# Kernel optimization log

Measured on AMD Instinct MI355X. Metric: run time of the kernel, lower is better.

Reference implementation:

```python
import jax, jax.numpy as jnp
import numpy as np

N, C_IN, H, W = 32, 128, 56, 56
C_OUT, KH, KW = 256, 3, 3
STRIDE = (1, 1)
PAD = (1, 1)


def setup_inputs() -> dict:
    key = jax.random.key(0)
    k_x, k_w, k_b = jax.random.split(key, 3)
    x = jax.random.normal(k_x, (N, C_IN, H, W), dtype=jnp.float32)
    # kaiming_uniform-like scale for weight, uniform bias in [-1/sqrt(fan_in), 1/sqrt(fan_in)]
    fan_in = C_IN * KH * KW
    bound_w = float(np.sqrt(6.0 / ((1 + 5.0) * fan_in)))  # kaiming_uniform a=sqrt(5)
    weight = jax.random.uniform(k_w, (C_OUT, C_IN, KH, KW), dtype=jnp.float32,
                                minval=-bound_w, maxval=bound_w)
    bound_b = float(1.0 / np.sqrt(fan_in))
    bias = jax.random.uniform(k_b, (C_OUT,), dtype=jnp.float32,
                              minval=-bound_b, maxval=bound_b)
    return {"x": x, "weight": weight, "bias": bias}


def reference(x, weight, bias):
    # Faithful math of the im2col conv: zero padding (ph,pw)=(1,1), stride 1,
    # groups=1 -> identical to a standard cross-correlation conv2d + bias.
    out = jax.lax.conv_general_dilated(
        x, weight,
        window_strides=STRIDE,
        padding=[(PAD[0], PAD[0]), (PAD[1], PAD[1])],
        dimension_numbers=("NCHW", "OIHW", "NCHW"),
    )
    return out + bias[None, :, None, None]
```

## Files before the change

### kernel.cpp

```cpp
#include <hip/hip_runtime.h>


#define NB   32
#define CIN  128
#define HH   56
#define WWD  56
#define COUT 256
#define HWP  3136
#define KTOT 1152
#define HP   58
#define XTN  (HP*HP*CIN)

typedef __bf16 bf16x8 __attribute__((ext_vector_type(8)));
typedef float  f32x4  __attribute__((ext_vector_type(4)));
typedef unsigned short u16;
typedef u16 u16x4 __attribute__((ext_vector_type(4)));
typedef u16 u16x8 __attribute__((ext_vector_type(8)));

__device__ __forceinline__ u16 f2b(float f) {
  unsigned u = __float_as_uint(f);
  u += 0x7fffu + ((u >> 16) & 1u);
  return (u16)(u >> 16);
}

__device__ __forceinline__ void load_lds16(const u16* g, u16* l) {
  __builtin_amdgcn_global_load_lds(
      (const __attribute__((address_space(1))) unsigned int*)g,
      (__attribute__((address_space(3))) unsigned int*)l, 16, 0, 0);
}

__global__ __launch_bounds__(256) void k_transpose_x(const float* __restrict__ x,
                                                     u16* __restrict__ xt) {
  __shared__ u16 tile[64][68];
  const int n  = blockIdx.z;
  const int p0 = blockIdx.x * 64;
  const int c0 = blockIdx.y * 64;
  const int t  = threadIdx.x;

  const float* xp = x + (size_t)n * CIN * HWP + (size_t)c0 * HWP + p0;
  const int pl = (t & 15) * 4;
  const int cr = t >> 4;
#pragma unroll
  for (int j = 0; j < 4; ++j) {
    int c = cr + j * 16;
    f32x4 v = *(const f32x4*)&xp[(size_t)c * HWP + pl];
    u16x4 h;
    h[0] = f2b(v[0]); h[1] = f2b(v[1]); h[2] = f2b(v[2]); h[3] = f2b(v[3]);
    *(u16x4*)&tile[c][pl] = h;
  }
  __syncthreads();
  u16* xb = xt + (size_t)n * XTN + c0;
  const int ch = (t & 7) * 8;
  const int pr = t >> 3;
#pragma unroll
  for (int j = 0; j < 2; ++j) {
    int p  = pr + j * 32;
    int s  = p0 + p;
    int oh = s / WWD;
    int ow = s - oh * WWD;
    u16x8 o;
#pragma unroll
    for (int i = 0; i < 8; ++i) o[i] = tile[ch + i][p];
    *(u16x8*)&xb[((size_t)(oh + 1) * HP + (ow + 1)) * CIN + ch] = o;
  }
}

__global__ __launch_bounds__(256) void k_transform_w(const float* __restrict__ w,
                                                     u16* __restrict__ Wt,
                                                     u16* __restrict__ xt) {
  int o = blockIdx.x * 256 + threadIdx.x;
  if (o < COUT * KTOT) {
    int co  = o / KTOT;
    int rem = o - co * KTOT;
    int kk  = rem >> 7;
    int ci  = rem & 127;
    int kh  = kk / 3;
    int kw  = kk - kh * 3;
    Wt[o] = f2b(w[(((size_t)co * CIN + ci) * 3 + kh) * 3 + kw]);
  }
#pragma unroll
  for (int j = 0; j < 4; ++j) {
    unsigned e = (unsigned)o + j * 294912u;
    if (e < 933888u) {
      unsigned n  = e / 29184u;
      unsigned rm = e - n * 29184u;
      unsigned bp = rm >> 7;
      unsigned ch = rm & 127u;
      unsigned ih, iw;
      if (bp < 58u)       { ih = 0;  iw = bp; }
      else if (bp < 116u) { ih = 57; iw = bp - 58u; }
      else { unsigned c2 = bp - 116u; ih = 1u + (c2 >> 1); iw = (c2 & 1u) ? 57u : 0u; }
      xt[(((size_t)n * HP + ih) * HP + iw) * CIN + ch] = (u16)0;
    }
  }
}


#define RD_A(qm_) do { _Pragma("unroll") for (int kk = 0; kk < 2; ++kk) \
    { _Pragma("unroll") for (int ti = 0; ti < 4; ++ti) \
      a[kk][ti] = *(const bf16x8*)&lds[eA + (wm*128 + (qm_)*64 + ti*16 + r)*64 \
                                        + (((kk*4 + q) ^ r7))*8]; } } while (0)

#define RD_B(qn_) do { _Pragma("unroll") for (int kk = 0; kk < 2; ++kk) \
    { _Pragma("unroll") for (int tj = 0; tj < 2; ++tj) \
      b[kk][tj] = *(const bf16x8*)&lds[eB + (wn*64 + (qn_)*32 + tj*16 + r)*64 \
                                        + (((kk*4 + q) ^ r7))*8]; } } while (0)

#define MM(qm_, qn_) do { _Pragma("unroll") for (int kk = 0; kk < 2; ++kk) \
    { _Pragma("unroll") for (int ti = 0; ti < 4; ++ti) \
      { _Pragma("unroll") for (int tj = 0; tj < 2; ++tj) \
        acc[(qm_)*4 + ti][(qn_)*2 + tj] = __builtin_amdgcn_mfma_f32_16x16x32_bf16( \
            a[kk][ti], b[kk][tj], acc[(qm_)*4 + ti][(qn_)*2 + tj], 0, 0, 0); } } } while (0)

__global__ __launch_bounds__(512, 2) void k_conv_gemm(
    const u16* __restrict__ xt, const u16* __restrict__ Wt,
    const float* __restrict__ bias, float* __restrict__ out) {
  extern __shared__ u16 lds[];
  const int tid  = threadIdx.x;
  const int wave = tid >> 6;
  const int lane = tid & 63;
  const int m0   = blockIdx.x * 256;

  const int wm = wave >> 2;
  const int wn = wave & 3;
  const int r  = lane & 15;
  const int q  = lane >> 4;
  const int r7 = r & 7;

  const int rsub = lane >> 3;
  const int ps8  = ((lane & 7) ^ rsub) * 8;

  int pbA[4], pbB[4], ldo[4];
#pragma unroll
  for (int j = 0; j < 4; ++j) {
    const int rowb = wave * 8 + j * 64;
    const int m  = m0 + rowb + rsub;
    const int n  = m / HWP;
    const int s  = m - n * HWP;
    const int oh = s / WWD;
    const int ow = s - oh * WWD;
    pbA[j] = ((n * HP + oh) * HP + ow) * CIN + ps8;
    pbB[j] = (rowb + rsub) * KTOT + ps8;
    ldo[j] = rowb * 64;
  }
  float bias_r[4];
#pragma unroll
  for (int tj = 0; tj < 4; ++tj) bias_r[tj] = bias[wn * 64 + tj * 16 + r];

  f32x4 acc[8][4];
#pragma unroll
  for (int i = 0; i < 8; ++i)
#pragma unroll
    for (int jj = 0; jj < 4; ++jj) acc[i][jj] = (f32x4){0.f, 0.f, 0.f, 0.f};

#pragma unroll
  for (int j = 0; j < 4; ++j) load_lds16(Wt + pbB[j], &lds[49152 + ldo[j]]);
#pragma unroll
  for (int j = 0; j < 4; ++j) load_lds16(xt + pbA[j], &lds[0 + ldo[j]]);
#pragma unroll
  for (int j = 0; j < 4; ++j) load_lds16(xt + pbA[j] + 64, &lds[16384 + ldo[j]]);
  asm volatile("s_waitcnt vmcnt(4)" ::: "memory");
  __builtin_amdgcn_s_barrier();

  bf16x8 a[2][4], b[2][2];
  int bA = 0, bB = 0;

#pragma unroll 1
  for (int kt = 0; kt < 18; ++kt) {
    const int eA  = bA * 16384;
    const int eB  = 49152 + bB * 16384;
    const int sAo = (bA == 0) ? 32768 : (bA - 1) * 16384;
    const int sBo = 49152 + ((bB ^ 1) * 16384);
    const int koffB = (kt + 1) * 64;
    const int kt2  = kt + 2;
    const int ksp2 = kt2 >> 1;
    const int kh2  = (ksp2 >= 6) ? 2 : ((ksp2 >= 3) ? 1 : 0);
    const int kw2  = ksp2 - kh2 * 3;
    const int UA   = (kh2 * HP + kw2) * CIN + ((kt2 & 1) << 6);
    const bool doB = (kt < 17);
    const bool doA = (kt < 16);

    RD_A(0); RD_B(0);
    if (doB) { load_lds16(Wt + pbB[0] + koffB, &lds[sBo + ldo[0]]);
               load_lds16(Wt + pbB[1] + koffB, &lds[sBo + ldo[1]]); }
    __builtin_amdgcn_s_barrier();
    __builtin_amdgcn_s_setprio(1);
    MM(0, 0);
    __builtin_amdgcn_s_setprio(0);
    __builtin_amdgcn_s_barrier();

    RD_B(1);
    if (doB) { load_lds16(Wt + pbB[2] + koffB, &lds[sBo + ldo[2]]);
               load_lds16(Wt + pbB[3] + koffB, &lds[sBo + ldo[3]]); }
    __builtin_amdgcn_s_barrier();
    __builtin_amdgcn_s_setprio(1);
    MM(0, 1);
    __builtin_amdgcn_s_setprio(0);
    __builtin_amdgcn_s_barrier();

    RD_A(1);
    if (doA) { load_lds16(xt + pbA[0] + UA, &lds[sAo + ldo[0]]);
               load_lds16(xt + pbA[1] + UA, &lds[sAo + ldo[1]]); }
    __builtin_amdgcn_s_barrier();
    __builtin_amdgcn_s_setprio(1);
    MM(1, 1);
    __builtin_amdgcn_s_setprio(0);
    __builtin_amdgcn_s_barrier();

    RD_B(0);
    if (doA) { load_lds16(xt + pbA[2] + UA, &lds[sAo + ldo[2]]);
               load_lds16(xt + pbA[3] + UA, &lds[sAo + ldo[3]]); }
    if (kt < 16) { asm volatile("s_waitcnt vmcnt(4)" ::: "memory"); }
    else         { asm volatile("s_waitcnt vmcnt(0)" ::: "memory"); }
    __builtin_amdgcn_s_barrier();
    __builtin_amdgcn_s_setprio(1);
    MM(1, 0);
    __builtin_amdgcn_s_setprio(0);
    __builtin_amdgcn_s_barrier();

    bA = (bA == 2) ? 0 : bA + 1;
    bB ^= 1;
  }

#pragma unroll
  for (int ti = 0; ti < 8; ++ti) {
    const int m4 = m0 + wm * 128 + ti * 16 + q * 4;
    const int n  = m4 / HWP;
    const int s  = m4 - n * HWP;
    float* op = out + (size_t)n * COUT * HWP + s;
#pragma unroll
    for (int tj = 0; tj < 4; ++tj) {
      const int co = wn * 64 + tj * 16 + r;
      f32x4 v = acc[ti][tj];
      const float bv = bias_r[tj];
      v[0] += bv; v[1] += bv; v[2] += bv; v[3] += bv;
      *(f32x4*)(op + (size_t)co * HWP) = v;
    }
  }
}

extern "C" void kernel_launch(void* const* d_in, const int* in_sizes, int n_in,
                              void* d_out, int out_size, void* d_ws, size_t ws_size,
                              hipStream_t stream) {
  const float* x    = (const float*)d_in[0];
  const float* w    = (const float*)d_in[1];
  const float* bias = (const float*)d_in[2];
  float* out        = (float*)d_out;

  u16* xt = (u16*)d_ws;
  u16* Wt = xt + (size_t)NB * XTN;

  static bool attr_done = false;
  if (!attr_done) {
    hipFuncSetAttribute(reinterpret_cast<const void*>(k_conv_gemm),
                        hipFuncAttributeMaxDynamicSharedMemorySize, 163840);
    attr_done = true;
  }

  k_transform_w<<<dim3(1152), dim3(256), 0, stream>>>(w, Wt, xt);
  k_transpose_x<<<dim3(49, 2, 32), dim3(256), 0, stream>>>(x, xt);
  k_conv_gemm<<<dim3(392), dim3(512), 163840, stream>>>(xt, Wt, bias, out);
}
```

Measured before the change: 219.7 us.

## Shrink conv GEMM tiles to 128x128 with simple double-buffered pipeline

Replaces the 256x256-tile, 512-thread conv GEMM (triple-buffered A, 160KB dynamic LDS, fine-grained interleaved barriers and setprio) with 128x128 tiles on 256 threads. It uses a plain two-stage double buffer in 64KB static LDS and a swizzled block-to-tile mapping across 1568 blocks. This is meant to raise occupancy and wave count and simplify scheduling. The cost is less data reuse per tile, roughly doubled global/L2 traffic for X and W, and full vmcnt(0) waits that expose load latency.

```diff
diff --git a/kernel.cpp b/kernel.cpp
--- a/kernel.cpp
+++ b/kernel.cpp
@@ -96,141 +96,109 @@
 }
 
 
-#define RD_A(qm_) do { _Pragma("unroll") for (int kk = 0; kk < 2; ++kk) \
-    { _Pragma("unroll") for (int ti = 0; ti < 4; ++ti) \
-      a[kk][ti] = *(const bf16x8*)&lds[eA + (wm*128 + (qm_)*64 + ti*16 + r)*64 \
-                                        + (((kk*4 + q) ^ r7))*8]; } } while (0)
-
-#define RD_B(qn_) do { _Pragma("unroll") for (int kk = 0; kk < 2; ++kk) \
-    { _Pragma("unroll") for (int tj = 0; tj < 2; ++tj) \
-      b[kk][tj] = *(const bf16x8*)&lds[eB + (wn*64 + (qn_)*32 + tj*16 + r)*64 \
-                                        + (((kk*4 + q) ^ r7))*8]; } } while (0)
-
-#define MM(qm_, qn_) do { _Pragma("unroll") for (int kk = 0; kk < 2; ++kk) \
-    { _Pragma("unroll") for (int ti = 0; ti < 4; ++ti) \
-      { _Pragma("unroll") for (int tj = 0; tj < 2; ++tj) \
-        acc[(qm_)*4 + ti][(qn_)*2 + tj] = __builtin_amdgcn_mfma_f32_16x16x32_bf16( \
-            a[kk][ti], b[kk][tj], acc[(qm_)*4 + ti][(qn_)*2 + tj], 0, 0, 0); } } } while (0)
-
-__global__ __launch_bounds__(512, 2) void k_conv_gemm(
+__device__ __forceinline__ int uX_off(int kt) {
+  int ksp = kt >> 1;
+  int kh  = (ksp >= 6) ? 2 : ((ksp >= 3) ? 1 : 0);
+  int kw  = ksp - kh * 3;
+  return (kh * HP + kw) * CIN + ((kt & 1) << 6);
+}
+
+#define STG(buf_, uxo_, uwo_) do { _Pragma("unroll") \
+  for (int c = 0; c < 4; ++c) { \
+    load_lds16(Wt + pbW[c] + (uwo_), &lW[buf_][ldo[c]]); \
+    load_lds16(xt + pbX[c] + (uxo_), &lX[buf_][ldo[c]]); } } while (0)
+
+#define CMP(buf_) do { _Pragma("unroll") for (int kk = 0; kk < 2; ++kk) { \
+    bf16x8 a[4], b[4]; const int sw = ((kk * 4 + q) ^ r7) * 8; \
+    _Pragma("unroll") for (int ti = 0; ti < 4; ++ti) \
+      a[ti] = *(const bf16x8*)&lX[buf_][(wm + ti * 16 + r) * 64 + sw]; \
+    _Pragma("unroll") for (int tj = 0; tj < 4; ++tj) \
+      b[tj] = *(const bf16x8*)&lW[buf_][(wc + tj * 16 + r) * 64 + sw]; \
+    _Pragma("unroll") for (int ti = 0; ti < 4; ++ti) \
+      _Pragma("unroll") for (int tj = 0; tj < 4; ++tj) \
+        acc[ti][tj] = __builtin_amdgcn_mfma_f32_16x16x32_bf16( \
+            a[ti], b[tj], acc[ti][tj], 0, 0, 0); } } while (0)
+
+__global__ __launch_bounds__(256, 2) void k_conv_gemm(
     const u16* __restrict__ xt, const u16* __restrict__ Wt,
     const float* __restrict__ bias, float* __restrict__ out) {
-  extern __shared__ u16 lds[];
+  __shared__ u16 lW[2][8192];
+  __shared__ u16 lX[2][8192];
+
   const int tid  = threadIdx.x;
   const int wave = tid >> 6;
   const int lane = tid & 63;
-  const int m0   = blockIdx.x * 256;
-
-  const int wm = wave >> 2;
-  const int wn = wave & 3;
+
+  const int bid  = blockIdx.x;
+  const int orig = (bid & 7) * 196 + (bid >> 3);
+  const int by   = orig / 784;
+  const int bx   = orig - by * 784;
+  const int m0   = bx * 128;
+  const int co0  = by * 128;
+
   const int r  = lane & 15;
   const int q  = lane >> 4;
   const int r7 = r & 7;
+  const int wm = (wave & 1) * 64;
+  const int wc = (wave >> 1) * 64;
 
   const int rsub = lane >> 3;
-  const int ps8  = ((lane & 7) ^ rsub) * 8;
-
-  int pbA[4], pbB[4], ldo[4];
-#pragma unroll
-  for (int j = 0; j < 4; ++j) {
-    const int rowb = wave * 8 + j * 64;
+  const int pso  = ((lane & 7) ^ rsub) * 8;
+
+  int pbX[4], pbW[4], ldo[4];
+#pragma unroll
+  for (int c = 0; c < 4; ++c) {
+    const int rowb = wave * 32 + c * 8;
     const int m  = m0 + rowb + rsub;
     const int n  = m / HWP;
     const int s  = m - n * HWP;
     const int oh = s / WWD;
     const int ow = s - oh * WWD;
-    pbA[j] = ((n * HP + oh) * HP + ow) * CIN + ps8;
-    pbB[j] = (rowb + rsub) * KTOT + ps8;
-    ldo[j] = rowb * 64;
+    pbX[c] = ((n * HP + oh) * HP + ow) * CIN + pso;
+    pbW[c] = (co0 + rowb + rsub) * KTOT + pso;
+    ldo[c] = rowb * 64;
   }
   float bias_r[4];
 #pragma unroll
-  for (int tj = 0; tj < 4; ++tj) bias_r[tj] = bias[wn * 64 + tj * 16 + r];
-
-  f32x4 acc[8][4];
-#pragma unroll
-  for (int i = 0; i < 8; ++i)
-#pragma unroll
-    for (int jj = 0; jj < 4; ++jj) acc[i][jj] = (f32x4){0.f, 0.f, 0.f, 0.f};
-
-#pragma unroll
-  for (int j = 0; j < 4; ++j) load_lds16(Wt + pbB[j], &lds[49152 + ldo[j]]);
-#pragma unroll
-  for (int j = 0; j < 4; ++j) load_lds16(xt + pbA[j], &lds[0 + ldo[j]]);
-#pragma unroll
-  for (int j = 0; j < 4; ++j) load_lds16(xt + pbA[j] + 64, &lds[16384 + ldo[j]]);
-  asm volatile("s_waitcnt vmcnt(4)" ::: "memory");
+  for (int tj = 0; tj < 4; ++tj) bias_r[tj] = bias[co0 + wc + tj * 16 + r];
+
+  f32x4 acc[4][4];
+#pragma unroll
+  for (int i = 0; i < 4; ++i)
+#pragma unroll
+    for (int j = 0; j < 4; ++j) acc[i][j] = (f32x4){0.f, 0.f, 0.f, 0.f};
+
+  STG(0, 0, 0);
+  asm volatile("s_waitcnt vmcnt(0)" ::: "memory");
   __builtin_amdgcn_s_barrier();
 
-  bf16x8 a[2][4], b[2][2];
-  int bA = 0, bB = 0;
-
 #pragma unroll 1
-  for (int kt = 0; kt < 18; ++kt) {
-    const int eA  = bA * 16384;
-    const int eB  = 49152 + bB * 16384;
-    const int sAo = (bA == 0) ? 32768 : (bA - 1) * 16384;
-    const int sBo = 49152 + ((bB ^ 1) * 16384);
-    const int koffB = (kt + 1) * 64;
-    const int kt2  = kt + 2;
-    const int ksp2 = kt2 >> 1;
-    const int kh2  = (ksp2 >= 6) ? 2 : ((ksp2 >= 3) ? 1 : 0);
-    const int kw2  = ksp2 - kh2 * 3;
-    const int UA   = (kh2 * HP + kw2) * CIN + ((kt2 & 1) << 6);
-    const bool doB = (kt < 17);
-    const bool doA = (kt < 16);
-
-    RD_A(0); RD_B(0);
-    if (doB) { load_lds16(Wt + pbB[0] + koffB, &lds[sBo + ldo[0]]);
-               load_lds16(Wt + pbB[1] + koffB, &lds[sBo + ldo[1]]); }
+  for (int p = 0; p < 8; ++p) {
+    const int kt = p * 2;
+    STG(1, uX_off(kt + 1), (kt + 1) * 64);
+    CMP(0);
+    asm volatile("s_waitcnt vmcnt(0)" ::: "memory");
     __builtin_amdgcn_s_barrier();
-    __builtin_amdgcn_s_setprio(1);
-    MM(0, 0);
-    __builtin_amdgcn_s_setprio(0);
+    STG(0, uX_off(kt + 2), (kt + 2) * 64);
+    CMP(1);
+    asm volatile("s_waitcnt vmcnt(0)" ::: "memory");
     __builtin_amdgcn_s_barrier();
-
-    RD_B(1);
-    if (doB) { load_lds16(Wt + pbB[2] + koffB, &lds[sBo + ldo[2]]);
-               load_lds16(Wt + pbB[3] + koffB, &lds[sBo + ldo[3]]); }
-    __builtin_amdgcn_s_barrier();
-    __builtin_amdgcn_s_setprio(1);
-    MM(0, 1);
-    __builtin_amdgcn_s_setprio(0);
-    __builtin_amdgcn_s_barrier();
-
-    RD_A(1);
-    if (doA) { load_lds16(xt + pbA[0] + UA, &lds[sAo + ldo[0]]);
-               load_lds16(xt + pbA[1] + UA, &lds[sAo + ldo[1]]); }
-    __builtin_amdgcn_s_barrier();
-    __builtin_amdgcn_s_setprio(1);
-    MM(1, 1);
-    __builtin_amdgcn_s_setprio(0);
-    __builtin_amdgcn_s_barrier();
-
-    RD_B(0);
-    if (doA) { load_lds16(xt + pbA[2] + UA, &lds[sAo + ldo[2]]);
-               load_lds16(xt + pbA[3] + UA, &lds[sAo + ldo[3]]); }
-    if (kt < 16) { asm volatile("s_waitcnt vmcnt(4)" ::: "memory"); }
-    else         { asm volatile("s_waitcnt vmcnt(0)" ::: "memory"); }
-    __builtin_amdgcn_s_barrier();
-    __builtin_amdgcn_s_setprio(1);
-    MM(1, 0);
-    __builtin_amdgcn_s_setprio(0);
-    __builtin_amdgcn_s_barrier();
-
-    bA = (bA == 2) ? 0 : bA + 1;
-    bB ^= 1;
-  }
-
-#pragma unroll
-  for (int ti = 0; ti < 8; ++ti) {
-    const int m4 = m0 + wm * 128 + ti * 16 + q * 4;
+  }
+  STG(1, uX_off(17), 17 * 64);
+  CMP(0);
+  asm volatile("s_waitcnt vmcnt(0)" ::: "memory");
+  __builtin_amdgcn_s_barrier();
+  CMP(1);
+
+#pragma unroll
+  for (int ti = 0; ti < 4; ++ti) {
+    const int m4 = m0 + wm + ti * 16 + q * 4;
     const int n  = m4 / HWP;
     const int s  = m4 - n * HWP;
     float* op = out + (size_t)n * COUT * HWP + s;
 #pragma unroll
     for (int tj = 0; tj < 4; ++tj) {
-      const int co = wn * 64 + tj * 16 + r;
+      const int co = co0 + wc + tj * 16 + r;
       f32x4 v = acc[ti][tj];
       const float bv = bias_r[tj];
       v[0] += bv; v[1] += bv; v[2] += bv; v[3] += bv;
@@ -250,14 +218,7 @@
   u16* xt = (u16*)d_ws;
   u16* Wt = xt + (size_t)NB * XTN;
 
-  static bool attr_done = false;
-  if (!attr_done) {
-    hipFuncSetAttribute(reinterpret_cast<const void*>(k_conv_gemm),
-                        hipFuncAttributeMaxDynamicSharedMemorySize, 163840);
-    attr_done = true;
-  }
-
   k_transform_w<<<dim3(1152), dim3(256), 0, stream>>>(w, Wt, xt);
   k_transpose_x<<<dim3(49, 2, 32), dim3(256), 0, stream>>>(x, xt);
-  k_conv_gemm<<<dim3(392), dim3(512), 163840, stream>>>(xt, Wt, bias, out);
-}
+  k_conv_gemm<<<dim3(1568), dim3(256), 0, stream>>>(xt, Wt, bias, out);
+}
```

New measurement: 218.8 us. About the same (-0.4%).
